# Performance work log

Measured on AMD Instinct MI355X. Metric: run time of the kernel, lower is better.

The kernel has to match this reference:

```python
import jax, jax.numpy as jnp
import numpy as np
from jax import lax

BN_EPS = 1e-5


def ste_sign(x):
    # binarize to {-1,+1} with straight-through estimator (BNN semantics)
    return x + lax.stop_gradient(jnp.where(x >= 0, 1.0, -1.0).astype(x.dtype) - x)


def _block(x, w, gamma, beta, pool):
    # IRPadding(1,1): pad spatial dims with -1 (binary '0' bit in hardware)
    x = jnp.pad(x, ((0, 0), (0, 0), (1, 1), (1, 1)), constant_values=-1.0)
    # IRConv2dFIN: sign-binarized weights, binary inputs, integer-valued output
    wb = ste_sign(w)
    x = lax.conv_general_dilated(x, wb, window_strides=(1, 1), padding='VALID',
                                 dimension_numbers=('NCHW', 'OIHW', 'NCHW'))
    # IRBatchNorm2d: per-channel batch-stat normalization with affine
    mean = jnp.mean(x, axis=(0, 2, 3), keepdims=True)
    var = jnp.var(x, axis=(0, 2, 3), keepdims=True)
    x = gamma[None, :, None, None] * (x - mean) * lax.rsqrt(var + BN_EPS) + beta[None, :, None, None]
    # Hardtanh then IRCLAP (sign clip to {-1,+1})
    x = jnp.clip(x, -1.0, 1.0)
    x = ste_sign(x)
    if pool:  # MaxPool2d(2,2)
        x = lax.reduce_window(x, -jnp.inf, lax.max, (1, 1, 2, 2), (1, 1, 2, 2), 'VALID')
    return x


def setup_inputs() -> dict:
    key = jax.random.key(0)
    ks = jax.random.split(key, 16)
    B = 256
    x = jnp.where(jax.random.normal(ks[0], (B, 3, 32, 32)) >= 0, 1.0, -1.0).astype(jnp.float32)
    chans = [(128, 3), (256, 128), (256, 256), (256, 256), (128, 256), (128, 128)]
    inp = {'x': x}
    for i, (co, ci) in enumerate(chans):
        n = 3 * 3 * co
        inp[f'w{i}'] = jax.random.normal(ks[1 + i], (co, ci, 3, 3), dtype=jnp.float32) * np.sqrt(2.0 / n)
        inp[f'g{i}'] = jnp.ones((co,), dtype=jnp.float32)
        inp[f'b{i}'] = jnp.zeros((co,), dtype=jnp.float32)
    inp['fc_w'] = jax.random.normal(ks[10], (10, 128 * 4 * 4), dtype=jnp.float32) * 0.01
    inp['fc_b'] = jnp.zeros((10,), dtype=jnp.float32)
    return inp


def reference(x, w0, g0, b0, w1, g1, b1, w2, g2, b2, w3, g3, b3, w4, g4, b4, w5, g5, b5, fc_w, fc_b):
    ws = [w0, w1, w2, w3, w4, w5]
    gs = [g0, g1, g2, g3, g4, g5]
    bs = [b0, b1, b2, b3, b4, b5]
    pools = [False, True, False, True, False, True]
    h = x
    for w, g, b, p in zip(ws, gs, bs, pools):
        h = _block(h, w, g, b, p)
    # flatten (dropout is identity at inference) -> fc
    h = h.reshape(h.shape[0], -1)  # [B, 128*4*4]
    return h @ fc_w.T + fc_b
```

## Files before the change

kernel.cpp:

```cpp
#include <hip/hip_runtime.h>
#include <stdint.h>

typedef unsigned long long ull;
typedef int i32x4 __attribute__((ext_vector_type(4)));
typedef int i32x16 __attribute__((ext_vector_type(16)));
#define BB 256

static const size_t OFF_CONV  = 0;
static const size_t OFF_ACT1  = 67108864;
static const size_t OFF_ACT2  = 104988672;
static const size_t OFF_BITS4 = 126222336;
static const size_t OFF_BITS5 = 127041536;
static const size_t OFF_WBPC  = 127451136;
static const size_t OFF_WPK   = 127506432;
static const size_t OFF_S     = 128980992;
static const size_t OFF_SS    = 128987136;
static const size_t OFF_ATHR  = 128999424;
static const size_t OFF_BTHR  = 129005568;
static const size_t OFF_H     = 129011712;
static const size_t OFF_XB    = 131108864;
static const size_t WS_NEEDED = 131207680;

#define SWZA(o) ((o) ^ (((((o) >> 7) ^ ((o) >> 10)) & 7) << 4))


__global__ void zero_stats_k(int* __restrict__ S, ull* __restrict__ SS) {
  int i = blockIdx.x * blockDim.x + threadIdx.x;
  if (i < 6 * 256) { S[i] = 0; SS[i] = 0ull; }
}

__global__ void pack_w_k(const float* __restrict__ w, uint32_t* __restrict__ out,
                         int co, int ci) {
  int K32 = ci >> 5;
  int total = 9 * K32 * co;
  int idx = blockIdx.x * blockDim.x + threadIdx.x;
  if (idx >= total) return;
  int c  = idx % co;
  int tk = idx / co;
  int k  = tk % K32;
  int t  = tk / K32;
  uint32_t word = 0;
  const float* wc = w + (size_t)c * ci * 9 + t;
  for (int j = 0; j < 32; ++j)
    if (wc[(size_t)(k * 32 + j) * 9] >= 0.f) word |= (1u << j);
  out[idx] = word;
}

__global__ void pack_wmfma_k(const float* __restrict__ w, signed char* __restrict__ out,
                             int co, int ci) {
  int KT = ci >> 5;
  int total = (co >> 5) * 9 * KT * 64;
  int idx = blockIdx.x * blockDim.x + threadIdx.x;
  if (idx >= total) return;
  int l   = idx & 63;
  int ctk = idx >> 6;
  int kt  = ctk % KT; int tmp = ctk / KT;
  int t   = tmp % 9;  int ct  = tmp / 9;
  int co_ = ct * 32 + (l & 31);
  int ci0 = kt * 32 + (l >> 5) * 16;
  const float* wp = w + ((size_t)co_ * ci + ci0) * 9 + t;
  int dw[4];
#pragma unroll
  for (int jj = 0; jj < 4; ++jj) {
    uint32_t d = 0;
#pragma unroll
    for (int bb = 0; bb < 4; ++bb) {
      float f = wp[(size_t)(jj * 4 + bb) * 9];
      d |= ((f >= 0.f) ? 0x01u : 0xFFu) << (8 * bb);
    }
    dw[jj] = (int)d;
  }
  *(i32x4*)(out + (size_t)idx * 16) = *(i32x4*)&dw[0];
}

__global__ void pack_x_k(const float* __restrict__ x, uint32_t* __restrict__ xbits) {
  int idx = blockIdx.x * 256 + threadIdx.x;
  if (idx >= 24576) return;
  const float* xp = x + (size_t)idx * 32;
  uint32_t w = 0;
#pragma unroll
  for (int j = 0; j < 32; ++j) if (xp[j] >= 0.f) w |= (1u << j);
  xbits[idx] = w;
}

__global__ void pack_w0_k(const float* __restrict__ w0, uint32_t* __restrict__ w27) {
  int co = threadIdx.x;
  uint32_t w = 0;
#pragma unroll
  for (int t = 0; t < 27; ++t) if (w0[co * 27 + t] >= 0.f) w |= (1u << t);
  w27[co] = w;
}

__global__ void __launch_bounds__(256) conv0x_k(
    const uint32_t* __restrict__ xbits, const uint32_t* __restrict__ w27,
    short* __restrict__ convout, int* __restrict__ Sg, ull* __restrict__ SSg) {
  int b  = blockIdx.x >> 2;
  int rg = blockIdx.x & 3;
  __shared__ uint32_t a27s[256];
  __shared__ uint32_t wlds[128];
  __shared__ int sS[256], sSS[256];
  int tid = threadIdx.x;
  if (tid < 128) wlds[tid] = w27[tid];

  int p = rg * 256 + tid;
  int y = p >> 5, xx = p & 31;
  const uint32_t* xb = xbits + (size_t)b * 96;
  uint32_t a27 = 0;
#pragma unroll
  for (int c = 0; c < 3; ++c)
#pragma unroll
    for (int kh = 0; kh < 3; ++kh) {
      int iy = y + kh - 1;
      uint32_t r = (iy >= 0 && iy < 32) ? xb[c * 32 + iy] : 0u;
      uint32_t bits3 = (uint32_t)((((uint64_t)r) << 1) >> xx) & 7u;
      a27 |= bits3 << (c * 9 + kh * 3);
    }
  a27s[tid] = a27;
  __syncthreads();

  int co = tid & 127, half = tid >> 7;
  uint32_t wv = wlds[co];
  int S = 0, SS = 0;
  int base = rg * 256 + half * 128;
  short* cb = convout + ((size_t)b * 1024 + base) * 128 + co;
  for (int i = 0; i < 128; ++i) {
    uint32_t a = a27s[half * 128 + i];
    int v = 27 - 2 * __popc(a ^ wv);
    S += v; SS += v * v;
    cb[(size_t)i * 128] = (short)v;
  }
  sS[tid] = S; sSS[tid] = SS;
  __syncthreads();
  if (tid < 128) {
    atomicAdd(&Sg[tid], sS[tid] + sS[tid + 128]);
    atomicAdd(&SSg[tid], (ull)(long long)(sSS[tid] + sSS[tid + 128]));
  }
}

__global__ void finalize_k(const int* __restrict__ S, const ull* __restrict__ SS,
                           int* __restrict__ A, int* __restrict__ B,
                           const float* __restrict__ gamma, const float* __restrict__ beta,
                           int co, int N) {
  int c = threadIdx.x;
  if (c >= co) return;
  double m  = (double)S[c] / (double)N;
  double e2 = (double)SS[c] / (double)N;
  double inv = 1.0 / sqrt(e2 - m * m + 1e-5);
  float gg = gamma[c], bb = beta[c];
  int Ai, Bi;
  if (gg > 0.f) {
    double t = m - (double)bb / ((double)gg * inv);
    t = fmin(fmax(t, -1e6), 1e6);
    Ai = 1;  Bi = (int)ceil(t);
  } else if (gg < 0.f) {
    double t = m - (double)bb / ((double)gg * inv);
    t = fmin(fmax(t, -1e6), 1e6);
    Ai = -1; Bi = -(int)floor(t);
  } else {
    Ai = 0;  Bi = (bb >= 0.f) ? 0 : 1;
  }
  A[c] = Ai; B[c] = Bi;
}

__global__ void binarize_k(const short* __restrict__ conv, int co, int H, int W, int pool,
                           uint32_t* __restrict__ out_bits, signed char* __restrict__ out8,
                           const int* __restrict__ A, const int* __restrict__ B,
                           float* __restrict__ hout) {
  __shared__ int As[256], Bs[256];
  int tid = threadIdx.x;
  for (int i = tid; i < co; i += 256) { As[i] = A[i]; Bs[i] = B[i]; }
  __syncthreads();

  int K32 = co >> 5;
  int Ho = pool ? (H >> 1) : H, Wo = pool ? (W >> 1) : W;
  int PH = Ho + 2, PW = Wo + 2;
  int total = BB * K32 * PH * PW;
  int idx = blockIdx.x * 256 + tid;
  if (idx >= total) return;
  int k  = idx % K32;
  int t1 = idx / K32;
  int px = t1 % PW; int t2 = t1 / PW;
  int py = t2 % PH; int b  = t2 / PH;
  uint32_t word = 0;
  if (py >= 1 && py <= Ho && px >= 1 && px <= Wo) {
    int oy = py - 1, ox = px - 1;
    int np = pool ? 2 : 1;
    for (int dy = 0; dy < np; ++dy)
      for (int dx = 0; dx < np; ++dx) {
        int iy = oy * np + dy, ix = ox * np + dx;
        const short* cp = conv + ((size_t)((b * H + iy) * W + ix)) * co + k * 32;
#pragma unroll
        for (int j = 0; j < 32; ++j) {
          int v = cp[j];
          int c = k * 32 + j;
          if (As[c] * v >= Bs[c]) word |= (1u << j);
        }
      }
    if (hout) {
#pragma unroll
      for (int j = 0; j < 32; ++j) {
        int c = k * 32 + j;
        hout[((size_t)(b * 128 + c) * 4 + oy) * 4 + ox] = ((word >> j) & 1) ? 1.f : -1.f;
      }
    }
  }
  if (out_bits)
    out_bits[((size_t)(b * K32 + k) * PH + py) * PW + px] = word;
  if (out8) {
    int dw[8];
#pragma unroll
    for (int jj = 0; jj < 8; ++jj) {
      uint32_t d = 0;
#pragma unroll
      for (int bb = 0; bb < 4; ++bb)
        d |= (((word >> (jj * 4 + bb)) & 1) ? 0x01u : 0xFFu) << (8 * bb);
      dw[jj] = (int)d;
    }
    signed char* p = out8 + (((size_t)(b * PH + py)) * PW + px) * (size_t)co + k * 32;
    *(i32x4*)p = *(i32x4*)&dw[0];
    *(i32x4*)(p + 16) = *(i32x4*)&dw[4];
  }
}

template <int CI, int W>
__global__ __launch_bounds__(256, 2) void conv_mfma_k(
    const signed char* __restrict__ act, const i32x4* __restrict__ wpk,
    short* __restrict__ convout, int* __restrict__ Sg, ull* __restrict__ SSg) {
  constexpr int KT = CI / 32;
  constexpr int PW = W + 2;
  constexpr int TR = 32 / W;
  constexpr int ROWS_BLK = 4 * TR;
  constexpr int NBY = W / ROWS_BLK;
  constexpr int AROWS = ROWS_BLK + 2;
  constexpr int ABYTES = AROWS * PW * CI;
  constexpr int NSTEP = 9 * KT;
  constexpr int NC = NSTEP / 4;

  __shared__ __attribute__((aligned(16))) char ldsA[ABYTES];

  int tid = threadIdx.x;
  int b = blockIdx.x / NBY, blk_y = blockIdx.x % NBY;
  int y0 = blk_y * ROWS_BLK;

  const signed char* src = act + ((size_t)b * (W + 2) + y0) * PW * CI;
  for (int o = tid * 16; o < ABYTES; o += 4096) {
    i32x4 v = *(const i32x4*)(src + o);
    *(i32x4*)(ldsA + SWZA(o)) = v;
  }
  __syncthreads();

  int l = tid & 63, w = tid >> 6;
  int wm = w & 1, wn = w >> 1;
  int r = l & 31, khalf = l >> 5;
  int px = (TR == 1) ? r : (r & 15);

  int inv[2];
#pragma unroll
  for (int m = 0; m < 2; ++m) {
    int ti = wm * 2 + m;
    int row = (TR == 1) ? ti : (ti * 2 + (r >> 4));
    inv[m] = (row * PW + px) * CI + khalf * 16;
  }
  const i32x4* wl = wpk + l;

  i32x16 acc[2][2];
#pragma unroll
  for (int m = 0; m < 2; ++m)
#pragma unroll
    for (int n = 0; n < 2; ++n)
#pragma unroll
      for (int q = 0; q < 16; ++q) acc[m][n][q] = 0;

  i32x4 bA[2][4], bB[2][4];

#define PB(buf, c)                                                             \
  if ((c) < NC) {                                                              \
    _Pragma("unroll") for (int ph = 0; ph < 4; ++ph) {                         \
      int s = (c) * 4 + ph; int t = s / KT, kt = s % KT;                       \
      _Pragma("unroll") for (int n = 0; n < 2; ++n)                            \
        buf[n][ph] = wl[(size_t)(((wn * 2 + n) * 9 + t) * KT + kt) * 64];      \
    }                                                                          \
  }

#define DC(buf, c)                                                             \
  {                                                                            \
    _Pragma("unroll") for (int ph = 0; ph < 4; ++ph) {                         \
      int s = (c) * 4 + ph; int t = s / KT, kt = s % KT;                       \
      int soff = ((t / 3) * PW + (t % 3)) * CI + kt * 32;                      \
      i32x4 a0, a1;                                                            \
      { int o = SWZA(inv[0] + soff); a0 = *(const i32x4*)(ldsA + o); }         \
      { int o = SWZA(inv[1] + soff); a1 = *(const i32x4*)(ldsA + o); }         \
      _Pragma("unroll") for (int n = 0; n < 2; ++n) {                          \
        acc[0][n] = __builtin_amdgcn_mfma_i32_32x32x32_i8(a0, buf[n][ph], acc[0][n], 0, 0, 0); \
        acc[1][n] = __builtin_amdgcn_mfma_i32_32x32x32_i8(a1, buf[n][ph], acc[1][n], 0, 0, 0); \
      }                                                                        \
    }                                                                          \
  }

  PB(bA, 0);
  for (int c = 0; c < NC; c += 2) {
    PB(bB, c + 1);
    DC(bA, c);
    PB(bA, c + 2);
    if (c + 1 < NC) DC(bB, c + 1);
  }
#undef PB
#undef DC

#pragma unroll
  for (int n = 0; n < 2; ++n) {
    int s1 = 0, s2 = 0;
#pragma unroll
    for (int m = 0; m < 2; ++m) {
      int ti = wm * 2 + m;
      i32x16 v = acc[m][n];
      int pk[8];
#pragma unroll
      for (int q = 0; q < 8; ++q) {
        int v0 = v[2 * q], v1 = v[2 * q + 1];
        s1 += v0 + v1; s2 += v0 * v0 + v1 * v1;
        pk[q] = (v0 & 0xffff) | (v1 << 16);
      }
      int fragLocal = ti * 4 + wn * 2 + n;
      size_t baseS = (((size_t)blockIdx.x * 16 + fragLocal) * 64 + l) * 16;
      *(i32x4*)(convout + baseS) = *(i32x4*)&pk[0];
      *(i32x4*)(convout + baseS + 8) = *(i32x4*)&pk[4];
    }
    s1 += __shfl_xor(s1, 32);
    s2 += __shfl_xor(s2, 32);
    if (l < 32) {
      int ch = wn * 64 + n * 32 + l;
      atomicAdd(&Sg[ch], s1);
      atomicAdd(&SSg[ch], (ull)(long long)s2);
    }
  }
}

template <int CO_BLK, int W, int POOL, int OUT_BITS, int OUTP, int K32TOT>
__global__ __launch_bounds__(256) void binarize_frag_k(
    const short* __restrict__ convout, signed char* __restrict__ out8,
    uint32_t* __restrict__ out_bits, const int* __restrict__ Ath,
    const int* __restrict__ Bth, int co_base) {
  constexpr int TR = 32 / W;
  constexpr int ROWS_BLK = 4 * TR;
  constexpr int NBY = W / ROWS_BLK;
  constexpr int K32B = CO_BLK / 32;
  constexpr int NT = CO_BLK / 64;
  constexpr int Wout = POOL ? W / 2 : W;
  constexpr int HoutB = POOL ? ROWS_BLK / 2 : ROWS_BLK;
  constexpr int WORDS = HoutB * Wout * K32B;
  constexpr int NP = POOL ? 2 : 1;
  constexpr int LBYTES = 128 * CO_BLK * 2;

  __shared__ __attribute__((aligned(16))) char ldsC[LBYTES];
  int tid = threadIdx.x;
  int b = blockIdx.x / NBY, blk_y = blockIdx.x % NBY;

  const char* src = (const char*)(convout + (size_t)blockIdx.x * (128 * CO_BLK));
  for (int o = tid * 16; o < LBYTES; o += 4096) {
    i32x4 v = *(const i32x4*)(src + o);
    int so = o ^ (((o >> 11) & 7) << 4);
    *(i32x4*)(ldsC + so) = v;
  }
  __syncthreads();

  for (int widx = tid; widx < WORDS; widx += 256) {
    int k = widx % K32B, opx = widx / K32B;
    int oy = opx / Wout, ox = opx % Wout;
    int wn = k / NT, n = k % NT;
    int bases[NP * NP];
#pragma unroll
    for (int dy = 0; dy < NP; ++dy)
#pragma unroll
      for (int dx = 0; dx < NP; ++dx) {
        int yl = POOL ? oy * 2 + dy : oy;
        int x  = POOL ? ox * 2 + dx : ox;
        int ti = yl / TR;
        int rr = (TR == 1) ? x : ((yl & 1) * 16 + x);
        int hi = (rr >> 2) & 1, q = (rr & 3) + 4 * (rr >> 3);
        int fragLocal = ti * K32B + wn * NT + n;
        bases[dy * NP + dx] = ((fragLocal * 64 + hi * 32) * 16 + q) * 2;
      }
    uint32_t word = 0;
    for (int j = 0; j < 32; ++j) {
      int c = k * 32 + j;
      int Aj = Ath[c], Bj = Bth[c];
      int mx = -0x7fffffff;
#pragma unroll
      for (int p2 = 0; p2 < NP * NP; ++p2) {
        int bo = bases[p2] + j * 32;
        bo ^= ((bo >> 11) & 7) << 4;
        int v = *(const short*)(ldsC + bo);
        int av = Aj * v;
        mx = (av > mx) ? av : mx;
      }
      if (mx >= Bj) word |= (1u << j);
    }
    int gy = blk_y * HoutB + oy, gx = ox;
    if (OUT_BITS) {
      out_bits[(((size_t)b * K32TOT + (co_base >> 5) + k) * OUTP + 1 + gy) * OUTP + 1 + gx] = word;
    } else {
      size_t a0 = (((size_t)b * OUTP + (1 + gy)) * OUTP + (1 + gx)) * 256 + co_base + k * 32;
      int dw[8];
#pragma unroll
      for (int jj = 0; jj < 8; ++jj) {
        uint32_t d = 0;
#pragma unroll
        for (int bb = 0; bb < 4; ++bb)
          d |= (((word >> (jj * 4 + bb)) & 1) ? 0x01u : 0xFFu) << (8 * bb);
        dw[jj] = (int)d;
      }
      *(i32x4*)(out8 + a0) = *(i32x4*)&dw[0];
      *(i32x4*)(out8 + a0 + 16) = *(i32x4*)&dw[4];
    }
  }
}

template <int K32>
__global__ void __launch_bounds__(256) conv_xnor_k(
    const uint32_t* __restrict__ act, const uint32_t* __restrict__ wb,
    short* __restrict__ convout, int* __restrict__ Sg, ull* __restrict__ SSg,
    int co, int H, int Ktot) {
  int Hp  = H + 2;
  int T   = H >> 3;
  int cot = co >> 6;
  int TT  = T * T * cot;
  int b   = blockIdx.x / TT;
  int r   = blockIdx.x % TT;
  int ct  = r % cot;
  int tt  = r / cot;
  int ty  = tt / T, tx = tt % T;
  int co_base = ct << 6;

  __shared__ __attribute__((aligned(16))) uint32_t ldsA[K32 * 10 * 12];
  __shared__ __attribute__((aligned(16))) uint32_t ldsB[9 * K32 * 64];
  __shared__ int sS[64];
  __shared__ int sSS[64];

  int tid = threadIdx.x;
  if (tid < 64) { sS[tid] = 0; sSS[tid] = 0; }
  for (int i = tid; i < 9 * K32 * 64; i += 256) {
    int c  = i & 63;
    int tk = i >> 6;
    ldsB[i] = wb[(size_t)tk * co + co_base + c];
  }
  const uint32_t* ab = act + (size_t)b * K32 * Hp * Hp;
  for (int i = tid; i < K32 * 100; i += 256) {
    int k  = i / 100;
    int rr = i % 100;
    int yy = rr / 10, xx = rr % 10;
    ldsA[(k * 10 + yy) * 12 + xx] = ab[(size_t)(k * Hp + ty * 8 + yy) * Hp + tx * 8 + xx];
  }
  __syncthreads();

  int tc   = tid & 15;
  int pgp  = tid >> 4;
  int yrow = pgp >> 1;
  int xg   = pgp & 1;

  int acc[4][4];
#pragma unroll
  for (int i = 0; i < 4; ++i)
#pragma unroll
    for (int j = 0; j < 4; ++j) acc[i][j] = 0;

#pragma unroll 1
  for (int k = 0; k < K32; ++k) {
#pragma unroll
    for (int kh = 0; kh < 3; ++kh) {
      int abase = (k * 10 + yrow + kh) * 12 + xg * 4;
      uint4 a0 = *(const uint4*)&ldsA[abase];
      uint2 a1 = *(const uint2*)&ldsA[abase + 4];
      uint32_t arow[6] = {a0.x, a0.y, a0.z, a0.w, a1.x, a1.y};
#pragma unroll
      for (int kw = 0; kw < 3; ++kw) {
        int t = kh * 3 + kw;
        uint4 bwv = *(const uint4*)&ldsB[(t * K32 + k) * 64 + tc * 4];
        uint32_t bwa[4] = {bwv.x, bwv.y, bwv.z, bwv.w};
#pragma unroll
        for (int pi = 0; pi < 4; ++pi) {
          uint32_t aw = arow[pi + kw];
#pragma unroll
          for (int cj = 0; cj < 4; ++cj)
            acc[pi][cj] += __popc(aw ^ bwa[cj]);
        }
      }
    }
  }

  int vS[4] = {0, 0, 0, 0}, vSS[4] = {0, 0, 0, 0};
  int gy0 = ty * 8 + yrow, gx0 = tx * 8 + xg * 4;
#pragma unroll
  for (int pi = 0; pi < 4; ++pi) {
    short4 vv;
    int v0 = Ktot - 2 * acc[pi][0];
    int v1 = Ktot - 2 * acc[pi][1];
    int v2 = Ktot - 2 * acc[pi][2];
    int v3 = Ktot - 2 * acc[pi][3];
    vS[0] += v0; vSS[0] += v0 * v0;
    vS[1] += v1; vSS[1] += v1 * v1;
    vS[2] += v2; vSS[2] += v2 * v2;
    vS[3] += v3; vSS[3] += v3 * v3;
    vv.x = (short)v0; vv.y = (short)v1; vv.z = (short)v2; vv.w = (short)v3;
    size_t obase = ((size_t)(b * H + gy0) * H + (gx0 + pi)) * co + co_base + tc * 4;
    *(short4*)&convout[obase] = vv;
  }
#pragma unroll
  for (int cj = 0; cj < 4; ++cj) {
    atomicAdd(&sS[tc * 4 + cj], vS[cj]);
    atomicAdd(&sSS[tc * 4 + cj], vSS[cj]);
  }
  __syncthreads();
  if (tid < 64) {
    atomicAdd(&Sg[co_base + tid], sS[tid]);
    atomicAdd(&SSg[co_base + tid], (ull)(long long)sSS[tid]);
  }
}

__global__ void fc_k(const float* __restrict__ h, const float* __restrict__ fcw,
                     const float* __restrict__ fcb, float* __restrict__ out) {
  int b = blockIdx.x;
  int tid = threadIdx.x;
  int j = tid & 15;
  int chunk = tid >> 4;
  __shared__ float red[16][17];
  float acc = 0.f;
  if (j < 10) {
    const float* hp = h + (size_t)b * 2048 + chunk * 128;
    const float* wp = fcw + (size_t)j * 2048 + chunk * 128;
    for (int i = 0; i < 128; ++i) acc += hp[i] * wp[i];
  }
  red[chunk][j] = acc;
  __syncthreads();
  if (tid < 10) {
    float s = fcb[tid];
    for (int c = 0; c < 16; ++c) s += red[c][tid];
    out[b * 10 + tid] = s;
  }
}


extern "C" void kernel_launch(void* const* d_in, const int* in_sizes, int n_in,
                              void* d_out, int out_size, void* d_ws, size_t ws_size,
                              hipStream_t stream) {
  (void)in_sizes; (void)n_in; (void)out_size;
  if (ws_size < WS_NEEDED) return;

  const float* x = (const float*)d_in[0];
  const float* w[6]; const float* g[6]; const float* bt[6];
  for (int i = 0; i < 6; ++i) {
    w[i]  = (const float*)d_in[1 + 3 * i];
    g[i]  = (const float*)d_in[2 + 3 * i];
    bt[i] = (const float*)d_in[3 + 3 * i];
  }
  const float* fcw = (const float*)d_in[19];
  const float* fcb = (const float*)d_in[20];

  char* ws = (char*)d_ws;
  short*        convout = (short*)(ws + OFF_CONV);
  signed char*  act1    = (signed char*)(ws + OFF_ACT1);
  signed char*  act2    = (signed char*)(ws + OFF_ACT2);
  uint32_t*     bits4   = (uint32_t*)(ws + OFF_BITS4);
  uint32_t*     bits5   = (uint32_t*)(ws + OFF_BITS5);
  uint32_t*     wbpc    = (uint32_t*)(ws + OFF_WBPC);
  signed char*  wpkc    = (signed char*)(ws + OFF_WPK);
  int*          Sg      = (int*)(ws + OFF_S);
  ull*          SSg     = (ull*)(ws + OFF_SS);
  int*          Athr    = (int*)(ws + OFF_ATHR);
  int*          Bthr    = (int*)(ws + OFF_BTHR);
  float*        hbuf    = (float*)(ws + OFF_H);
  uint32_t*     xbits   = (uint32_t*)(ws + OFF_XB);
  uint32_t*     w27     = xbits + 24576;
  float*        out     = (float*)d_out;

  const i32x4* wpk1 = (const i32x4*)wpkc;
  const i32x4* wpk2 = wpk1 + 294912 / 16;
  const i32x4* wpk3 = wpk1 + 884736 / 16;

  zero_stats_k<<<6, 256, 0, stream>>>(Sg, SSg);

  pack_w_k<<<36, 256, 0, stream>>>(w[4], wbpc, 128, 256);
  pack_w_k<<<18, 256, 0, stream>>>(w[5], wbpc + 9216, 128, 128);
  pack_wmfma_k<<<72, 256, 0, stream>>>(w[1], wpkc, 256, 128);
  pack_wmfma_k<<<144, 256, 0, stream>>>(w[2], wpkc + 294912, 256, 256);
  pack_wmfma_k<<<144, 256, 0, stream>>>(w[3], wpkc + 884736, 256, 256);
  pack_x_k<<<96, 256, 0, stream>>>(x, xbits);
  pack_w0_k<<<1, 128, 0, stream>>>(w[0], w27);

  hipMemsetAsync(act2, 0xFF, 21233664, stream);
  hipMemsetAsync(bits4, 0x00, 819200, stream);

  conv0x_k<<<256 * 4, 256, 0, stream>>>(xbits, w27, convout, Sg, SSg);
  finalize_k<<<1, 256, 0, stream>>>(Sg, SSg, Athr, Bthr, g[0], bt[0], 128, 262144);
  binarize_k<<<(256 * 4 * 34 * 34 + 255) / 256, 256, 0, stream>>>(
      convout, 128, 32, 32, 0, nullptr, act1, Athr, Bthr, nullptr);

  conv_mfma_k<128, 32><<<2048, 256, 0, stream>>>(act1, wpk1, convout, Sg + 256, SSg + 256);
  finalize_k<<<1, 256, 0, stream>>>(Sg + 256, SSg + 256, Athr + 256, Bthr + 256, g[1], bt[1], 128, 262144);
  binarize_frag_k<128, 32, 1, 0, 18, 8><<<2048, 256, 0, stream>>>(
      convout, act2, nullptr, Athr + 256, Bthr + 256, 0);

  conv_mfma_k<128, 32><<<2048, 256, 0, stream>>>(act1, wpk1 + 9216, convout, Sg + 384, SSg + 384);
  finalize_k<<<1, 256, 0, stream>>>(Sg + 384, SSg + 384, Athr + 384, Bthr + 384, g[1] + 128, bt[1] + 128, 128, 262144);
  hipMemsetAsync(act1, 0xFF, 21233664, stream);
  binarize_frag_k<128, 32, 1, 0, 18, 8><<<2048, 256, 0, stream>>>(
      convout, act2, nullptr, Athr + 384, Bthr + 384, 128);

  conv_mfma_k<256, 16><<<512, 256, 0, stream>>>(act2, wpk2, convout, Sg + 512, SSg + 512);
  finalize_k<<<1, 256, 0, stream>>>(Sg + 512, SSg + 512, Athr + 512, Bthr + 512, g[2], bt[2], 128, 65536);
  binarize_frag_k<128, 16, 0, 0, 18, 8><<<512, 256, 0, stream>>>(
      convout, act1, nullptr, Athr + 512, Bthr + 512, 0);

  conv_mfma_k<256, 16><<<512, 256, 0, stream>>>(act2, wpk2 + 18432, convout, Sg + 640, SSg + 640);
  finalize_k<<<1, 256, 0, stream>>>(Sg + 640, SSg + 640, Athr + 640, Bthr + 640, g[2] + 128, bt[2] + 128, 128, 65536);
  binarize_frag_k<128, 16, 0, 0, 18, 8><<<512, 256, 0, stream>>>(
      convout, act1, nullptr, Athr + 640, Bthr + 640, 128);

  conv_mfma_k<256, 16><<<512, 256, 0, stream>>>(act1, wpk3, convout, Sg + 768, SSg + 768);
  finalize_k<<<1, 256, 0, stream>>>(Sg + 768, SSg + 768, Athr + 768, Bthr + 768, g[3], bt[3], 128, 65536);
  binarize_frag_k<128, 16, 1, 1, 10, 8><<<512, 256, 0, stream>>>(
      convout, nullptr, bits4, Athr + 768, Bthr + 768, 0);

  conv_mfma_k<256, 16><<<512, 256, 0, stream>>>(act1, wpk3 + 18432, convout, Sg + 896, SSg + 896);
  finalize_k<<<1, 256, 0, stream>>>(Sg + 896, SSg + 896, Athr + 896, Bthr + 896, g[3] + 128, bt[3] + 128, 128, 65536);
  binarize_frag_k<128, 16, 1, 1, 10, 8><<<512, 256, 0, stream>>>(
      convout, nullptr, bits4, Athr + 896, Bthr + 896, 128);

  conv_xnor_k<8><<<256 * 2, 256, 0, stream>>>(bits4, wbpc, convout,
                                              Sg + 1024, SSg + 1024, 128, 8, 2304);
  finalize_k<<<1, 256, 0, stream>>>(Sg + 1024, SSg + 1024, Athr + 1024, Bthr + 1024, g[4], bt[4], 128, 16384);
  binarize_k<<<(256 * 4 * 10 * 10 + 255) / 256, 256, 0, stream>>>(
      convout, 128, 8, 8, 0, bits5, nullptr, Athr + 1024, Bthr + 1024, nullptr);

  conv_xnor_k<4><<<256 * 2, 256, 0, stream>>>(bits5, wbpc + 9216, convout,
                                              Sg + 1280, SSg + 1280, 128, 8, 1152);
  finalize_k<<<1, 256, 0, stream>>>(Sg + 1280, SSg + 1280, Athr + 1280, Bthr + 1280, g[5], bt[5], 128, 16384);
  binarize_k<<<(256 * 4 * 6 * 6 + 255) / 256, 256, 0, stream>>>(
      convout, 128, 8, 8, 1, bits4, nullptr, Athr + 1280, Bthr + 1280, hbuf);

  fc_k<<<256, 256, 0, stream>>>(hbuf, fcw, fcb, out);
}
```

Measured before the change: 652.4 us.

## Drop LDS staging in int8 MFMA conv, load activations directly from global

```diff
diff --git a/kernel.cpp b/kernel.cpp
--- a/kernel.cpp
+++ b/kernel.cpp
@@ -20,8 +20,6 @@
 static const size_t OFF_H     = 129011712;
 static const size_t OFF_XB    = 131108864;
 static const size_t WS_NEEDED = 131207680;
-
-#define SWZA(o) ((o) ^ (((((o) >> 7) ^ ((o) >> 10)) & 7) << 4))
 
 
 __global__ void zero_stats_k(int* __restrict__ S, ull* __restrict__ SS) {
@@ -223,7 +221,7 @@
 }
 
 template <int CI, int W>
-__global__ __launch_bounds__(256, 2) void conv_mfma_k(
+__global__ __launch_bounds__(256, 3) void conv_mfma_k(
     const signed char* __restrict__ act, const i32x4* __restrict__ wpk,
     short* __restrict__ convout, int* __restrict__ Sg, ull* __restrict__ SSg) {
   constexpr int KT = CI / 32;
@@ -231,35 +229,23 @@
   constexpr int TR = 32 / W;
   constexpr int ROWS_BLK = 4 * TR;
   constexpr int NBY = W / ROWS_BLK;
-  constexpr int AROWS = ROWS_BLK + 2;
-  constexpr int ABYTES = AROWS * PW * CI;
   constexpr int NSTEP = 9 * KT;
-  constexpr int NC = NSTEP / 4;
-
-  __shared__ __attribute__((aligned(16))) char ldsA[ABYTES];
 
   int tid = threadIdx.x;
   int b = blockIdx.x / NBY, blk_y = blockIdx.x % NBY;
   int y0 = blk_y * ROWS_BLK;
-
-  const signed char* src = act + ((size_t)b * (W + 2) + y0) * PW * CI;
-  for (int o = tid * 16; o < ABYTES; o += 4096) {
-    i32x4 v = *(const i32x4*)(src + o);
-    *(i32x4*)(ldsA + SWZA(o)) = v;
-  }
-  __syncthreads();
 
   int l = tid & 63, w = tid >> 6;
   int wm = w & 1, wn = w >> 1;
   int r = l & 31, khalf = l >> 5;
   int px = (TR == 1) ? r : (r & 15);
 
-  int inv[2];
+  const signed char* abase[2];
 #pragma unroll
   for (int m = 0; m < 2; ++m) {
     int ti = wm * 2 + m;
     int row = (TR == 1) ? ti : (ti * 2 + (r >> 4));
-    inv[m] = (row * PW + px) * CI + khalf * 16;
+    abase[m] = act + (((size_t)b * (W + 2) + y0 + row) * PW + px) * CI + khalf * 16;
   }
   const i32x4* wl = wpk + l;
 
@@ -271,41 +257,19 @@
 #pragma unroll
       for (int q = 0; q < 16; ++q) acc[m][n][q] = 0;
 
-  i32x4 bA[2][4], bB[2][4];
-
-#define PB(buf, c)                                                             \
-  if ((c) < NC) {                                                              \
-    _Pragma("unroll") for (int ph = 0; ph < 4; ++ph) {                         \
-      int s = (c) * 4 + ph; int t = s / KT, kt = s % KT;                       \
-      _Pragma("unroll") for (int n = 0; n < 2; ++n)                            \
-        buf[n][ph] = wl[(size_t)(((wn * 2 + n) * 9 + t) * KT + kt) * 64];      \
-    }                                                                          \
-  }
-
-#define DC(buf, c)                                                             \
-  {                                                                            \
-    _Pragma("unroll") for (int ph = 0; ph < 4; ++ph) {                         \
-      int s = (c) * 4 + ph; int t = s / KT, kt = s % KT;                       \
-      int soff = ((t / 3) * PW + (t % 3)) * CI + kt * 32;                      \
-      i32x4 a0, a1;                                                            \
-      { int o = SWZA(inv[0] + soff); a0 = *(const i32x4*)(ldsA + o); }         \
-      { int o = SWZA(inv[1] + soff); a1 = *(const i32x4*)(ldsA + o); }         \
-      _Pragma("unroll") for (int n = 0; n < 2; ++n) {                          \
-        acc[0][n] = __builtin_amdgcn_mfma_i32_32x32x32_i8(a0, buf[n][ph], acc[0][n], 0, 0, 0); \
-        acc[1][n] = __builtin_amdgcn_mfma_i32_32x32x32_i8(a1, buf[n][ph], acc[1][n], 0, 0, 0); \
-      }                                                                        \
-    }                                                                          \
-  }
-
-  PB(bA, 0);
-  for (int c = 0; c < NC; c += 2) {
-    PB(bB, c + 1);
-    DC(bA, c);
-    PB(bA, c + 2);
-    if (c + 1 < NC) DC(bB, c + 1);
-  }
-#undef PB
-#undef DC
+#pragma unroll
+  for (int s = 0; s < NSTEP; ++s) {
+    const int t = s / KT, kt = s % KT;
+    const int aoff = ((t / 3) * PW + (t % 3)) * CI + kt * 32;
+    i32x4 a0 = *(const i32x4*)(abase[0] + aoff);
+    i32x4 a1 = *(const i32x4*)(abase[1] + aoff);
+    i32x4 b0 = wl[(size_t)(((wn * 2 + 0) * 9 + t) * KT + kt) * 64];
+    i32x4 b1 = wl[(size_t)(((wn * 2 + 1) * 9 + t) * KT + kt) * 64];
+    acc[0][0] = __builtin_amdgcn_mfma_i32_32x32x32_i8(a0, b0, acc[0][0], 0, 0, 0);
+    acc[0][1] = __builtin_amdgcn_mfma_i32_32x32x32_i8(a0, b1, acc[0][1], 0, 0, 0);
+    acc[1][0] = __builtin_amdgcn_mfma_i32_32x32x32_i8(a1, b0, acc[1][0], 0, 0, 0);
+    acc[1][1] = __builtin_amdgcn_mfma_i32_32x32x32_i8(a1, b1, acc[1][1], 0, 0, 0);
+  }
 
 #pragma unroll
   for (int n = 0; n < 2; ++n) {
```

Result: slower. 861.4 us (+32.0%).
